# Kernel tuning notes

Measured on AMD Instinct MI355X. Metric: run time of the kernel, lower is better.

## Reference

```python
import jax, jax.numpy as jnp
import numpy as np

N_P, E_P = 50000, 400000
N_L, E_L = 50000, 400000
B = 256  # number of graphs per side
NEG_GAT = 0.2   # GATv2 leaky-relu slope
NEG_FC = 0.01   # nn.LeakyReLU default slope


def _gatv2(x, ei, Wl, Wr, att, b, H, C):
    """GATv2Conv (concat heads, add_self_loops=True). Wl/Wr: [in, H*C], att: [H, C], b: [H*C]."""
    N = x.shape[0]
    sl = jnp.arange(N)
    src = jnp.concatenate([ei[0], sl])
    dst = jnp.concatenate([ei[1], sl])
    xl = (x @ Wl).reshape(N, H, C)   # source transform (messages)
    xr = (x @ Wr).reshape(N, H, C)   # target transform
    e = jax.nn.leaky_relu(xl[src] + xr[dst], NEG_GAT)          # [E+N, H, C]
    logits = jnp.einsum('ehc,hc->eh', e, att)                   # [E+N, H]
    m = jax.ops.segment_max(logits, dst, num_segments=N)        # segment softmax
    a = jnp.exp(logits - m[dst])
    alpha = a / jax.ops.segment_sum(a, dst, num_segments=N)[dst]
    out = jax.ops.segment_sum(xl[src] * alpha[..., None], dst, num_segments=N)
    return out.reshape(N, H * C) + b


def _mean_pool(x, batch, nb):
    s = jax.ops.segment_sum(x, batch, num_segments=nb)
    c = jax.ops.segment_sum(jnp.ones((x.shape[0],), x.dtype), batch, num_segments=nb)
    return s / jnp.maximum(c, 1.0)[:, None]


def setup_inputs() -> dict:
    key = jax.random.key(0)
    ks = jax.random.split(key, 48)
    i = [0]
    def nrm(shape, fan_in):
        k = ks[i[0]]; i[0] += 1
        return jax.random.normal(k, shape, jnp.float32) / np.sqrt(fan_in)
    inp = {}
    inp['protein_x'] = jax.random.normal(ks[40], (N_P, 10), jnp.float32)
    inp['ligand_x'] = jax.random.normal(ks[41], (N_L, 5), jnp.float32)
    inp['protein_edge_index'] = jax.random.randint(ks[42], (2, E_P), 0, N_P)
    inp['ligand_edge_index'] = jax.random.randint(ks[43], (2, E_L), 0, N_L)
    inp['protein_batch'] = (jnp.arange(N_P) * B) // N_P  # sorted graph ids, all segments nonempty
    inp['ligand_batch'] = (jnp.arange(N_L) * B) // N_L
    # GATv2 params: layer1 heads=2 out=128, layer2 heads=1 out=256
    inp['p1_Wl'] = nrm((10, 256), 10); inp['p1_Wr'] = nrm((10, 256), 10)
    inp['p1_att'] = nrm((2, 128), 128); inp['p1_b'] = jnp.zeros((256,), jnp.float32)
    inp['p2_Wl'] = nrm((256, 256), 256); inp['p2_Wr'] = nrm((256, 256), 256)
    inp['p2_att'] = nrm((1, 256), 256); inp['p2_b'] = jnp.zeros((256,), jnp.float32)
    inp['l1_Wl'] = nrm((5, 256), 5); inp['l1_Wr'] = nrm((5, 256), 5)
    inp['l1_att'] = nrm((2, 128), 128); inp['l1_b'] = jnp.zeros((256,), jnp.float32)
    inp['l2_Wl'] = nrm((256, 256), 256); inp['l2_Wr'] = nrm((256, 256), 256)
    inp['l2_att'] = nrm((1, 256), 256); inp['l2_b'] = jnp.zeros((256,), jnp.float32)
    # MultiheadAttention(256, 4) params ([in, out] convention)
    inp['Wq'] = nrm((256, 256), 256); inp['bq'] = jnp.zeros((256,), jnp.float32)
    inp['Wk'] = nrm((256, 256), 256); inp['bk'] = jnp.zeros((256,), jnp.float32)
    inp['Wv'] = nrm((256, 256), 256); inp['bv'] = jnp.zeros((256,), jnp.float32)
    inp['Wo'] = nrm((256, 256), 256); inp['bo'] = jnp.zeros((256,), jnp.float32)
    # fc head
    inp['fc1_w'] = nrm((512, 256), 512); inp['fc1_b'] = jnp.zeros((256,), jnp.float32)
    inp['ln_g'] = jnp.ones((256,), jnp.float32); inp['ln_b'] = jnp.zeros((256,), jnp.float32)
    inp['fc2_w'] = nrm((256, 1), 256); inp['fc2_b'] = jnp.zeros((1,), jnp.float32)
    return inp


def reference(protein_x, protein_edge_index, protein_batch,
              ligand_x, ligand_edge_index, ligand_batch,
              p1_Wl, p1_Wr, p1_att, p1_b, p2_Wl, p2_Wr, p2_att, p2_b,
              l1_Wl, l1_Wr, l1_att, l1_b, l2_Wl, l2_Wr, l2_att, l2_b,
              Wq, bq, Wk, bk, Wv, bv, Wo, bo,
              fc1_w, fc1_b, ln_g, ln_b, fc2_w, fc2_b):
    px = _gatv2(protein_x, protein_edge_index, p1_Wl, p1_Wr, p1_att, p1_b, 2, 128)
    px = _gatv2(px, protein_edge_index, p2_Wl, p2_Wr, p2_att, p2_b, 1, 256)
    px = _mean_pool(px, protein_batch, B)                        # [B, 256]
    lx = _gatv2(ligand_x, ligand_edge_index, l1_Wl, l1_Wr, l1_att, l1_b, 2, 128)
    lx = _gatv2(lx, ligand_edge_index, l2_Wl, l2_Wr, l2_att, l2_b, 1, 256)
    lx = _mean_pool(lx, ligand_batch, B)                         # [B, 256]
    # cross attention with q/k/v seq length 1
    D, H = 256, 4
    d = D // H
    qh = (px @ Wq + bq).reshape(B, H, d)
    kh = (lx @ Wk + bk).reshape(B, H, d)
    vh = (lx @ Wv + bv).reshape(B, H, d)
    scores = (qh * kh).sum(-1) / jnp.sqrt(jnp.float32(d))        # [B, H], 1 key
    w = jax.nn.softmax(scores[..., None], axis=-1)               # all ones (single key)
    attn = (w * vh).reshape(B, D) @ Wo + bo                      # [B, 256]
    comb = jnp.concatenate([px, attn], axis=1)                   # [B, 512]
    h = comb @ fc1_w + fc1_b
    mu = h.mean(-1, keepdims=True)
    var = h.var(-1, keepdims=True)
    h = (h - mu) / jnp.sqrt(var + 1e-5) * ln_g + ln_b
    h = jax.nn.leaky_relu(h, NEG_FC)
    return h @ fc2_w + fc2_b                                     # [B, 1]
```

## Files before the change

kernel.cpp:

```cpp
#include <hip/hip_runtime.h>
#include <math.h>

typedef unsigned short u16;
typedef __attribute__((ext_vector_type(8))) short bf16x8;
typedef __attribute__((ext_vector_type(4))) float f32x4;

__device__ inline u16 f2bf(float x) {
  unsigned int u = __float_as_uint(x);
  u += 0x7fffu + ((u >> 16) & 1u);
  return (u16)(u >> 16);
}
__device__ inline float bf2f(u16 h) {
  return __uint_as_float(((unsigned int)h) << 16);
}
__device__ inline float4 ld_bf4(const u16* p) {
  ushort4 v = *(const ushort4*)p;
  return make_float4(bf2f(v.x), bf2f(v.y), bf2f(v.z), bf2f(v.w));
}

__global__ void k_setup(int* __restrict__ cnt, int nz,
                        const float* __restrict__ Wpl, const float* __restrict__ Wpr,
                        const float* __restrict__ Wll, const float* __restrict__ Wlr,
                        u16* __restrict__ Whp, u16* __restrict__ Wlp,
                        u16* __restrict__ Whl, u16* __restrict__ Wll_o) {
  const int zb = (nz + 255) / 256;
  if ((int)blockIdx.x < zb) {
    int i = blockIdx.x * 256 + threadIdx.x;
    if (i < nz) cnt[i] = 0;
    return;
  }
  int wb = blockIdx.x - zb;
  int n = wb & 511;
  int side = wb >> 9;
  int col = n & 255;
  int k = threadIdx.x;
  const float* W = side == 0 ? (n < 256 ? Wpl : Wpr) : (n < 256 ? Wll : Wlr);
  float w = W[k * 256 + col];
  u16* Wh = side ? Whl : Whp;
  u16* Wlo = side ? Wll_o : Wlp;
  u16 hb = f2bf(w);
  Wh[n * 256 + k] = hb;
  Wlo[n * 256 + k] = f2bf(w - bf2f(hb));
}

__global__ void k_histb(const int* __restrict__ eip, int Ep, const int* __restrict__ eil,
                        int El, int* __restrict__ cntp, int* __restrict__ cntl) {
  int e = blockIdx.x * blockDim.x + threadIdx.x;
  if (e < Ep) atomicAdd(&cntp[eip[Ep + e]], 1);
  else if (e < Ep + El) { int e2 = e - Ep; atomicAdd(&cntl[eil[El + e2]], 1); }
}

__global__ void k_scan1b(const int* __restrict__ cntp, int Np, const int* __restrict__ cntl,
                         int Nl, int nbp, int* __restrict__ offsp, int* __restrict__ offsl,
                         int* __restrict__ curp, int* __restrict__ curl,
                         int* __restrict__ bsum) {
  __shared__ int s[256];
  int tid = threadIdx.x;
  int side = ((int)blockIdx.x >= nbp) ? 1 : 0;
  int blk = side ? (blockIdx.x - nbp) : blockIdx.x;
  const int* cnt = side ? cntl : cntp;
  int* offs = side ? offsl : offsp;
  int* cur = side ? curl : curp;
  int N = side ? Nl : Np;
  int i = blk * 256 + tid;
  int v = (i < N) ? cnt[i] : 0;
  if (i < N) cur[i] = 0;
  s[tid] = v;
  __syncthreads();
  for (int off = 1; off < 256; off <<= 1) {
    int t = 0;
    if (tid >= off) t = s[tid - off];
    __syncthreads();
    if (tid >= off) s[tid] += t;
    __syncthreads();
  }
  if (i < N) offs[i] = s[tid] - v;
  if (tid == 255) bsum[side * 256 + blk] = s[255];
}

__global__ void k_scan2b(int* __restrict__ bsum, int nbp, int nbl) {
  __shared__ int s[256];
  int side = blockIdx.x;
  int nb = side ? nbl : nbp;
  int* bs = bsum + side * 256;
  int tid = threadIdx.x;
  int v = (tid < nb) ? bs[tid] : 0;
  s[tid] = v;
  __syncthreads();
  for (int off = 1; off < 256; off <<= 1) {
    int t = 0;
    if (tid >= off) t = s[tid - off];
    __syncthreads();
    if (tid >= off) s[tid] += t;
    __syncthreads();
  }
  if (tid < nb) bs[tid] = s[tid] - v;
}

__global__ void k_fillb(const int* __restrict__ eip, int Ep, const int* __restrict__ eil,
                        int El, const int* __restrict__ offsp, const int* __restrict__ offsl,
                        const int* __restrict__ bsum,
                        int* __restrict__ curp, int* __restrict__ curl,
                        int* __restrict__ csrp, int* __restrict__ csrl) {
  int e = blockIdx.x * blockDim.x + threadIdx.x;
  if (e < Ep) {
    int d = eip[Ep + e];
    int pos = offsp[d] + bsum[d >> 8] + atomicAdd(&curp[d], 1);
    csrp[pos] = eip[e];
  } else if (e < Ep + El) {
    int e2 = e - Ep;
    int d = eil[El + e2];
    int pos = offsl[d] + bsum[256 + (d >> 8)] + atomicAdd(&curl[d], 1);
    csrl[pos] = eil[e2];
  }
}

__global__ void k_lin_small_b(const float* __restrict__ xp, int Kp, int Np,
                              const float* __restrict__ xl_, int Kl, int Nl,
                              const float* __restrict__ Wpl, const float* __restrict__ Wpr,
                              const float* __restrict__ Wll, const float* __restrict__ Wlr,
                              u16* __restrict__ xlh_p, u16* __restrict__ xrh_p,
                              u16* __restrict__ xlh_l, u16* __restrict__ xrh_l) {
  const int side = blockIdx.y;
  const float* x = side ? xl_ : xp;
  const int K = side ? Kl : Kp;
  const int N = side ? Nl : Np;
  const float* Wl = side ? Wll : Wpl;
  const float* Wr = side ? Wlr : Wpr;
  u16* xlh = side ? xlh_l : xlh_p;
  u16* xrh = side ? xrh_l : xrh_p;
  int base = blockIdx.x * 8;
  if (base >= N) return;
  int j = threadIdx.x;
  __shared__ float xs[8][16];
  int tot = 8 * K;
  for (int i = j; i < tot; i += 256) {
    int r = i / K, k = i - r * K;
    if (base + r < N) xs[r][k] = x[(size_t)(base + r) * K + k];
  }
  __syncthreads();
#pragma unroll
  for (int r = 0; r < 8; ++r) {
    int n = base + r;
    if (n >= N) break;
    float al = 0.f, ar = 0.f;
    for (int k = 0; k < K; ++k) {
      float xv = xs[r][k];
      al = fmaf(xv, Wl[k * 256 + j], al);
      ar = fmaf(xv, Wr[k * 256 + j], ar);
    }
    xlh[(size_t)n * 256 + j] = f2bf(al);
    xrh[(size_t)n * 256 + j] = f2bf(ar);
  }
}

__global__ void __launch_bounds__(256, 2) k_mm_dual_b(
    const u16* __restrict__ A_p, const u16* __restrict__ A_l,
    const u16* __restrict__ Bh_p, const u16* __restrict__ Bl_p,
    const u16* __restrict__ Bh_l, const u16* __restrict__ Bl_l,
    u16* __restrict__ XLh_p, u16* __restrict__ XRh_p,
    u16* __restrict__ XLh_l, u16* __restrict__ XRh_l, int Np, int Nl) {
  __shared__ __align__(16) char smem[32768];
  char* sA = smem;
  char* sBh = smem + 8192;
  char* sBl = smem + 16384;
  const int side = blockIdx.z;
  const u16* A = side ? A_l : A_p;
  const u16* Bhi = side ? Bh_l : Bh_p;
  const u16* Blo = side ? Bl_l : Bl_p;
  u16* XLh = side ? XLh_l : XLh_p;
  u16* XRh = side ? XRh_l : XRh_p;
  const int M = side ? Nl : Np;
  const int t = threadIdx.x;
  const int rowBase = blockIdx.x * 128;
  if (rowBase >= M) return;
  const int j0 = blockIdx.y * 128;
  const int srow = t >> 1;
  const int h = t & 1;
  int gr = rowBase + srow;
  if (gr >= M) gr = M - 1;
  const size_t gaBase = (size_t)gr * 256 + h * 16;
  const size_t gbBase = (size_t)(j0 + srow) * 256 + h * 16;
  const int rb = srow * 64;
  const int sw0 = (((h * 2) + (srow >> 1)) & 3) * 16;
  const int sw1 = (((h * 2 + 1) + (srow >> 1)) & 3) * 16;
  const int lane = t & 63;
  const int wid = t >> 6;
  const int wm = (wid & 1) * 64;
  const int wn = (wid >> 1) * 64;
  const int kq = lane >> 4;
  const int mr = lane & 15;
  int offA[4], offB[4];
#pragma unroll
  for (int i = 0; i < 4; ++i) {
    int m = wm + i * 16 + mr;
    offA[i] = m * 64 + ((kq + (m >> 1)) & 3) * 16;
    int n = wn + i * 16 + mr;
    offB[i] = n * 64 + ((kq + (n >> 1)) & 3) * 16;
  }
  f32x4 acc[4][4] = {};
  for (int kt = 0; kt < 8; ++kt) {
    const int k0 = kt * 32;
    uint4 va0 = *(const uint4*)(A + gaBase + k0);
    uint4 va1 = *(const uint4*)(A + gaBase + k0 + 8);
    uint4 vbh0 = *(const uint4*)(Bhi + gbBase + k0);
    uint4 vbh1 = *(const uint4*)(Bhi + gbBase + k0 + 8);
    uint4 vbl0 = *(const uint4*)(Blo + gbBase + k0);
    uint4 vbl1 = *(const uint4*)(Blo + gbBase + k0 + 8);
    __syncthreads();
    *(uint4*)(sA + rb + sw0) = va0;
    *(uint4*)(sA + rb + sw1) = va1;
    *(uint4*)(sBh + rb + sw0) = vbh0;
    *(uint4*)(sBh + rb + sw1) = vbh1;
    *(uint4*)(sBl + rb + sw0) = vbl0;
    *(uint4*)(sBl + rb + sw1) = vbl1;
    __syncthreads();
    bf16x8 a[4], bh[4], bl[4];
#pragma unroll
    for (int i = 0; i < 4; ++i) {
      a[i] = *(const bf16x8*)(sA + offA[i]);
      bh[i] = *(const bf16x8*)(sBh + offB[i]);
      bl[i] = *(const bf16x8*)(sBl + offB[i]);
    }
#pragma unroll
    for (int i = 0; i < 4; ++i)
#pragma unroll
      for (int j = 0; j < 4; ++j) {
        acc[i][j] = __builtin_amdgcn_mfma_f32_16x16x32_bf16(a[i], bh[j], acc[i][j], 0, 0, 0);
        acc[i][j] = __builtin_amdgcn_mfma_f32_16x16x32_bf16(a[i], bl[j], acc[i][j], 0, 0, 0);
      }
  }
  __syncthreads();
  u16* wtile = (u16*)(smem + wid * 8192);
#pragma unroll
  for (int i = 0; i < 4; ++i)
#pragma unroll
    for (int j = 0; j < 4; ++j)
#pragma unroll
      for (int r = 0; r < 4; ++r)
        wtile[(i * 16 + kq * 4 + r) * 64 + j * 16 + mr] = f2bf(acc[i][j][r]);
  u16* cbase = (blockIdx.y < 2) ? XLh : XRh;
  const int cb = (blockIdx.y < 2) ? j0 : j0 - 256;
  const int r8 = lane >> 3;
  const int c8 = lane & 7;
#pragma unroll
  for (int rr = 0; rr < 8; ++rr) {
    int lr = rr * 8 + r8;
    uint4 v = *(const uint4*)&wtile[lr * 64 + c8 * 8];
    int row = rowBase + wm + lr;
    if (row < M) *(uint4*)&cbase[(size_t)row * 256 + cb + wn + c8 * 8] = v;
  }
}

#define GAT_DOT(a, q)                                                          \
  {                                                                            \
    float t0 = a.x + rd.x, t1 = a.y + rd.y, t2 = a.z + rd.z, t3 = a.w + rd.w;  \
    q = fmaf(t3, wa6.w, fabsf(t3) * wa4.w);                                    \
    q = fmaf(fabsf(t2), wa4.z, fmaf(t2, wa6.z, q));                            \
    q = fmaf(fabsf(t1), wa4.y, fmaf(t1, wa6.y, q));                            \
    q = fmaf(fabsf(t0), wa4.x, fmaf(t0, wa6.x, q));                            \
  }

template <int H>
__global__ void k_gat_gather_b(
    const u16* __restrict__ xlh_p, const u16* __restrict__ xrh_p, u16* __restrict__ out_p,
    const u16* __restrict__ xlh_l, const u16* __restrict__ xrh_l, u16* __restrict__ out_l,
    const int* __restrict__ csr_p, const int* __restrict__ offs_p,
    const int* __restrict__ cnt_p,
    const int* __restrict__ csr_l, const int* __restrict__ offs_l,
    const int* __restrict__ cnt_l, const int* __restrict__ bsum,
    const float* __restrict__ att_p, const float* __restrict__ bias_p,
    const float* __restrict__ att_l, const float* __restrict__ bias_l,
    int Np, int Nl) {
  const int side = blockIdx.y;
  const u16* xlh = side ? xlh_l : xlh_p;
  const u16* xrh = side ? xrh_l : xrh_p;
  u16* out = side ? out_l : out_p;
  const int* csr = side ? csr_l : csr_p;
  const int* offs = side ? offs_l : offs_p;
  const int* cnt = side ? cnt_l : cnt_p;
  const float* att = side ? att_l : att_p;
  const float* bias = side ? bias_l : bias_p;
  const int N = side ? Nl : Np;
  int d = blockIdx.x * 4 + (threadIdx.x >> 6);
  if (d >= N) return;
  const int lo4 = (threadIdx.x & 63) * 4;
  const float4 rd = ld_bf4(&xrh[(size_t)d * 256 + lo4]);
  const float4 wa = *(const float4*)&att[lo4];
  const float4 wa6 = make_float4(0.6f * wa.x, 0.6f * wa.y, 0.6f * wa.z, 0.6f * wa.w);
  const float4 wa4 = make_float4(0.4f * wa.x, 0.4f * wa.y, 0.4f * wa.z, 0.4f * wa.w);
  const float4 xd = ld_bf4(&xlh[(size_t)d * 256 + lo4]);
  float base;
  GAT_DOT(xd, base)
#pragma unroll
  for (int off = 1; off <= (H == 2 ? 16 : 32); off <<= 1) base += __shfl_xor(base, off, 64);
  float l0 = 1.f, l1 = 0.f, l2 = 0.f, l3 = 0.f;
  float4 acc0 = xd;
  float4 acc1 = make_float4(0.f, 0.f, 0.f, 0.f);
  float4 acc2 = make_float4(0.f, 0.f, 0.f, 0.f);
  float4 acc3 = make_float4(0.f, 0.f, 0.f, 0.f);
  const int o0 = offs[d] + bsum[side * 256 + (d >> 8)];
  const int c = cnt[d];
  int j = 0;
  for (; j + 3 < c; j += 4) {
    int s0 = csr[o0 + j], s1 = csr[o0 + j + 1], s2 = csr[o0 + j + 2], s3 = csr[o0 + j + 3];
    float4 a0 = ld_bf4(&xlh[(size_t)s0 * 256 + lo4]);
    float4 a1 = ld_bf4(&xlh[(size_t)s1 * 256 + lo4]);
    float4 a2 = ld_bf4(&xlh[(size_t)s2 * 256 + lo4]);
    float4 a3 = ld_bf4(&xlh[(size_t)s3 * 256 + lo4]);
    float q0, q1, q2, q3;
    GAT_DOT(a0, q0)
    GAT_DOT(a1, q1)
    GAT_DOT(a2, q2)
    GAT_DOT(a3, q3)
#pragma unroll
    for (int off = 1; off <= (H == 2 ? 16 : 32); off <<= 1) {
      q0 += __shfl_xor(q0, off, 64);
      q1 += __shfl_xor(q1, off, 64);
      q2 += __shfl_xor(q2, off, 64);
      q3 += __shfl_xor(q3, off, 64);
    }
    float w0 = __expf(q0 - base), w1 = __expf(q1 - base);
    float w2 = __expf(q2 - base), w3 = __expf(q3 - base);
    l0 += w0; l1 += w1; l2 += w2; l3 += w3;
    acc0.x = fmaf(w0, a0.x, acc0.x); acc0.y = fmaf(w0, a0.y, acc0.y);
    acc0.z = fmaf(w0, a0.z, acc0.z); acc0.w = fmaf(w0, a0.w, acc0.w);
    acc1.x = fmaf(w1, a1.x, acc1.x); acc1.y = fmaf(w1, a1.y, acc1.y);
    acc1.z = fmaf(w1, a1.z, acc1.z); acc1.w = fmaf(w1, a1.w, acc1.w);
    acc2.x = fmaf(w2, a2.x, acc2.x); acc2.y = fmaf(w2, a2.y, acc2.y);
    acc2.z = fmaf(w2, a2.z, acc2.z); acc2.w = fmaf(w2, a2.w, acc2.w);
    acc3.x = fmaf(w3, a3.x, acc3.x); acc3.y = fmaf(w3, a3.y, acc3.y);
    acc3.z = fmaf(w3, a3.z, acc3.z); acc3.w = fmaf(w3, a3.w, acc3.w);
  }
  for (; j < c; ++j) {
    int s0 = csr[o0 + j];
    float4 a0 = ld_bf4(&xlh[(size_t)s0 * 256 + lo4]);
    float q0;
    GAT_DOT(a0, q0)
#pragma unroll
    for (int off = 1; off <= (H == 2 ? 16 : 32); off <<= 1) q0 += __shfl_xor(q0, off, 64);
    float w0 = __expf(q0 - base);
    l0 += w0;
    acc0.x = fmaf(w0, a0.x, acc0.x); acc0.y = fmaf(w0, a0.y, acc0.y);
    acc0.z = fmaf(w0, a0.z, acc0.z); acc0.w = fmaf(w0, a0.w, acc0.w);
  }
  float inv = 1.f / (l0 + l1 + l2 + l3);
  float ax = acc0.x + acc1.x + acc2.x + acc3.x;
  float ay = acc0.y + acc1.y + acc2.y + acc3.y;
  float az = acc0.z + acc1.z + acc2.z + acc3.z;
  float aw = acc0.w + acc1.w + acc2.w + acc3.w;
  const float4 b4 = *(const float4*)&bias[lo4];
  ushort4 hv;
  hv.x = f2bf(ax * inv + b4.x);
  hv.y = f2bf(ay * inv + b4.y);
  hv.z = f2bf(az * inv + b4.z);
  hv.w = f2bf(aw * inv + b4.w);
  *(ushort4*)&out[(size_t)d * 256 + lo4] = hv;
}

#define POOL_C 8
__global__ void k_pool_part(const u16* __restrict__ xp, const int* __restrict__ bp, int Np,
                            const u16* __restrict__ xl_, const int* __restrict__ bl_, int Nl,
                            float* __restrict__ PPpart, float* __restrict__ LPpart) {
  const int b = blockIdx.x;
  const int side = blockIdx.y;
  const int chunk = blockIdx.z;
  const u16* x = side ? xl_ : xp;
  const int* batch = side ? bl_ : bp;
  const int N = side ? Nl : Np;
  float* part = side ? LPpart : PPpart;
  int j = threadIdx.x;
  __shared__ int sss, sse;
  if (j == 0) {
    int lo = 0, hi = N;
    while (lo < hi) { int mid = (lo + hi) >> 1; if (batch[mid] < b) lo = mid + 1; else hi = mid; }
    sss = lo;
    lo = 0; hi = N;
    while (lo < hi) { int mid = (lo + hi) >> 1; if (batch[mid] < b + 1) lo = mid + 1; else hi = mid; }
    sse = lo;
  }
  __syncthreads();
  int len = sse - sss;
  int per = (len + POOL_C - 1) / POOL_C;
  int st = sss + chunk * per;
  int en = st + per;
  if (en > sse) en = sse;
  float acc = 0.f;
  for (int n = st; n < en; ++n) acc += bf2f(x[(size_t)n * 256 + j]);
  part[((size_t)chunk * 256 + b) * 256 + j] = acc;
}

__global__ void k_head(const float* __restrict__ PPpart, const float* __restrict__ LPpart,
                       const int* __restrict__ bp, int Np,
                       const int* __restrict__ bl_, int Nl,
                       const float* __restrict__ Wv, const float* __restrict__ bv,
                       const float* __restrict__ Wo, const float* __restrict__ bo,
                       const float* __restrict__ fc1w, const float* __restrict__ fc1b,
                       const float* __restrict__ lng, const float* __restrict__ lnb,
                       const float* __restrict__ fc2w, const float* __restrict__ fc2b,
                       float* __restrict__ out) {
  int b = blockIdx.x;
  int j = threadIdx.x;
  __shared__ float lxs[256];
  __shared__ float vbuf[256];
  __shared__ float comb[512];
  __shared__ float r1[256], r2[256];
  __shared__ float smu, srs;
  __shared__ int seg[4];
  if (j < 2) {
    const int* batch = j ? bl_ : bp;
    int N = j ? Nl : Np;
    int lo = 0, hi = N;
    while (lo < hi) { int mid = (lo + hi) >> 1; if (batch[mid] < b) lo = mid + 1; else hi = mid; }
    seg[j * 2] = lo;
    lo = 0; hi = N;
    while (lo < hi) { int mid = (lo + hi) >> 1; if (batch[mid] < b + 1) lo = mid + 1; else hi = mid; }
    seg[j * 2 + 1] = lo;
  }
  __syncthreads();
  {
    float accp = 0.f, accl = 0.f;
#pragma unroll
    for (int c = 0; c < POOL_C; ++c) {
      accp += PPpart[((size_t)c * 256 + b) * 256 + j];
      accl += LPpart[((size_t)c * 256 + b) * 256 + j];
    }
    comb[j] = accp / fmaxf((float)(seg[1] - seg[0]), 1.f);
    lxs[j] = accl / fmaxf((float)(seg[3] - seg[2]), 1.f);
  }
  __syncthreads();
  float v = bv[j];
  for (int k = 0; k < 256; ++k) v = fmaf(lxs[k], Wv[k * 256 + j], v);
  vbuf[j] = v;
  __syncthreads();
  float at = bo[j];
  for (int k = 0; k < 256; ++k) at = fmaf(vbuf[k], Wo[k * 256 + j], at);
  comb[256 + j] = at;
  __syncthreads();
  float h = fc1b[j];
  for (int k = 0; k < 512; ++k) h = fmaf(comb[k], fc1w[k * 256 + j], h);
  r1[j] = h;
  r2[j] = h * h;
  __syncthreads();
  for (int off = 128; off > 0; off >>= 1) {
    if (j < off) { r1[j] += r1[j + off]; r2[j] += r2[j + off]; }
    __syncthreads();
  }
  if (j == 0) {
    float mu = r1[0] / 256.f;
    float var = r2[0] / 256.f - mu * mu;
    smu = mu;
    srs = 1.f / sqrtf(var + 1e-5f);
  }
  __syncthreads();
  float hn = (h - smu) * srs * lng[j] + lnb[j];
  hn = hn > 0.f ? hn : 0.01f * hn;
  r1[j] = hn * fc2w[j];
  __syncthreads();
  for (int off = 128; off > 0; off >>= 1) {
    if (j < off) r1[j] += r1[j + off];
    __syncthreads();
  }
  if (j == 0) out[b] = r1[0] + fc2b[0];
}

extern "C" void kernel_launch(void* const* d_in, const int* in_sizes, int n_in,
                              void* d_out, int out_size, void* d_ws, size_t ws_size,
                              hipStream_t stream) {
  const float* px = (const float*)d_in[0];
  const float* lx = (const float*)d_in[1];
  const int* pei = (const int*)d_in[2];
  const int* lei = (const int*)d_in[3];
  const int* pb = (const int*)d_in[4];
  const int* lb = (const int*)d_in[5];
  const float* p1_Wl = (const float*)d_in[6];
  const float* p1_Wr = (const float*)d_in[7];
  const float* p1_att = (const float*)d_in[8];
  const float* p1_b = (const float*)d_in[9];
  const float* p2_Wl = (const float*)d_in[10];
  const float* p2_Wr = (const float*)d_in[11];
  const float* p2_att = (const float*)d_in[12];
  const float* p2_b = (const float*)d_in[13];
  const float* l1_Wl = (const float*)d_in[14];
  const float* l1_Wr = (const float*)d_in[15];
  const float* l1_att = (const float*)d_in[16];
  const float* l1_b = (const float*)d_in[17];
  const float* l2_Wl = (const float*)d_in[18];
  const float* l2_Wr = (const float*)d_in[19];
  const float* l2_att = (const float*)d_in[20];
  const float* l2_b = (const float*)d_in[21];
  const float* Wv = (const float*)d_in[26];
  const float* bv = (const float*)d_in[27];
  const float* Wo = (const float*)d_in[28];
  const float* bo = (const float*)d_in[29];
  const float* fc1w = (const float*)d_in[30];
  const float* fc1b = (const float*)d_in[31];
  const float* lng = (const float*)d_in[32];
  const float* lnb = (const float*)d_in[33];
  const float* fc2w = (const float*)d_in[34];
  const float* fc2b = (const float*)d_in[35];

  const int NPn = in_sizes[4];
  const int NLn = in_sizes[5];
  const int EPe = in_sizes[2] / 2;
  const int ELe = in_sizes[3] / 2;
  const int KP = in_sizes[0] / NPn;
  const int KL = in_sizes[1] / NLn;

  const int Nmax = NPn > NLn ? NPn : NLn;
  const int Emax = EPe > ELe ? EPe : ELe;
  size_t NF = (size_t)Nmax * 256;

  u16* XLh_p = (u16*)d_ws;
  u16* XRh_p = XLh_p + NF;
  u16* Ah_p = XRh_p + NF;
  u16* XLh_l = Ah_p + NF;
  u16* XRh_l = XLh_l + NF;
  u16* Ah_l = XRh_l + NF;
  u16* Wth = Ah_l + NF;
  u16* Wtl = Wth + 2 * 512 * 256;
  float* PPpart = (float*)(Wtl + 2 * 512 * 256);
  float* LPpart = PPpart + (size_t)POOL_C * 256 * 256;
  int* cnt = (int*)(LPpart + (size_t)POOL_C * 256 * 256);
  int* cur = cnt + 2 * (size_t)Nmax;
  int* offs = cur + 2 * (size_t)Nmax;
  int* bsum = offs + 2 * (size_t)Nmax;
  int* csr = bsum + 512;
  int* cnt_l = cnt + Nmax;
  int* cur_l = cur + Nmax;
  int* offs_l = offs + Nmax;
  int* csr_l = csr + Emax;

  const int nbp = (NPn + 255) / 256;
  const int nbl = (NLn + 255) / 256;
  const int nz = 2 * Nmax;
  const int zb = (nz + 255) / 256;

  k_setup<<<zb + 1024, 256, 0, stream>>>(cnt, nz, p2_Wl, p2_Wr, l2_Wl, l2_Wr,
                                         Wth, Wtl, Wth + 512 * 256, Wtl + 512 * 256);
  k_histb<<<(EPe + ELe + 255) / 256, 256, 0, stream>>>(pei, EPe, lei, ELe, cnt, cnt_l);
  k_scan1b<<<nbp + nbl, 256, 0, stream>>>(cnt, NPn, cnt_l, NLn, nbp, offs, offs_l,
                                          cur, cur_l, bsum);
  k_scan2b<<<2, 256, 0, stream>>>(bsum, nbp, nbl);
  k_fillb<<<(EPe + ELe + 255) / 256, 256, 0, stream>>>(pei, EPe, lei, ELe, offs, offs_l,
                                                       bsum, cur, cur_l, csr, csr_l);
  k_lin_small_b<<<dim3((Nmax + 7) / 8, 2), 256, 0, stream>>>(
      px, KP, NPn, lx, KL, NLn, p1_Wl, p1_Wr, l1_Wl, l1_Wr,
      XLh_p, XRh_p, XLh_l, XRh_l);
  k_gat_gather_b<2><<<dim3((Nmax + 3) / 4, 2), 256, 0, stream>>>(
      XLh_p, XRh_p, Ah_p, XLh_l, XRh_l, Ah_l,
      csr, offs, cnt, csr_l, offs_l, cnt_l, bsum,
      p1_att, p1_b, l1_att, l1_b, NPn, NLn);
  k_mm_dual_b<<<dim3((Nmax + 127) / 128, 4, 2), 256, 0, stream>>>(
      Ah_p, Ah_l, Wth, Wtl, Wth + 512 * 256, Wtl + 512 * 256,
      XLh_p, XRh_p, XLh_l, XRh_l, NPn, NLn);
  k_gat_gather_b<1><<<dim3((Nmax + 3) / 4, 2), 256, 0, stream>>>(
      XLh_p, XRh_p, Ah_p, XLh_l, XRh_l, Ah_l,
      csr, offs, cnt, csr_l, offs_l, cnt_l, bsum,
      p2_att, p2_b, l2_att, l2_b, NPn, NLn);
  k_pool_part<<<dim3(256, 2, POOL_C), 256, 0, stream>>>(Ah_p, pb, NPn, Ah_l, lb, NLn,
                                                        PPpart, LPpart);
  k_head<<<256, 256, 0, stream>>>(PPpart, LPpart, pb, NPn, lb, NLn,
                                  Wv, bv, Wo, bo, fc1w, fc1b, lng, lnb, fc2w, fc2b,
                                  (float*)d_out);
  (void)n_in; (void)out_size; (void)ws_size;
}
```

Baseline: 573.8 us.

## Fold layer-1 linear into setup kernel and group GEMM blocks for L2 reuse

Merges the small first-layer linear transform into the setup kernel as extra blocks, which removes one kernel launch. The dual GEMM launch changes from a 3D grid to a flat grid. Groups of 8 row tiles now share their 4 column tiles within 32 consecutive block ids, so A rows and B columns are reused from L2 while hot, and both sides share one padded row range. The trade-off is a larger, more divergent setup kernel and some index arithmetic in the GEMM.

```diff
diff --git a/kernel.cpp b/kernel.cpp
--- a/kernel.cpp
+++ b/kernel.cpp
@@ -19,10 +19,17 @@
 }
 
 __global__ void k_setup(int* __restrict__ cnt, int nz,
-                        const float* __restrict__ Wpl, const float* __restrict__ Wpr,
-                        const float* __restrict__ Wll, const float* __restrict__ Wlr,
+                        const float* __restrict__ W2pl, const float* __restrict__ W2pr,
+                        const float* __restrict__ W2ll, const float* __restrict__ W2lr,
                         u16* __restrict__ Whp, u16* __restrict__ Wlp,
-                        u16* __restrict__ Whl, u16* __restrict__ Wll_o) {
+                        u16* __restrict__ Whl, u16* __restrict__ Wll_o,
+                        const float* __restrict__ xp, int Kp, int Np,
+                        const float* __restrict__ xl_, int Kl, int Nl,
+                        const float* __restrict__ W1pl, const float* __restrict__ W1pr,
+                        const float* __restrict__ W1ll, const float* __restrict__ W1lr,
+                        u16* __restrict__ xlh_p, u16* __restrict__ xrh_p,
+                        u16* __restrict__ xlh_l, u16* __restrict__ xrh_l,
+                        int linPer) {
   const int zb = (nz + 255) / 256;
   if ((int)blockIdx.x < zb) {
     int i = blockIdx.x * 256 + threadIdx.x;
@@ -30,17 +37,52 @@
     return;
   }
   int wb = blockIdx.x - zb;
-  int n = wb & 511;
-  int side = wb >> 9;
-  int col = n & 255;
-  int k = threadIdx.x;
-  const float* W = side == 0 ? (n < 256 ? Wpl : Wpr) : (n < 256 ? Wll : Wlr);
-  float w = W[k * 256 + col];
-  u16* Wh = side ? Whl : Whp;
-  u16* Wlo = side ? Wll_o : Wlp;
-  u16 hb = f2bf(w);
-  Wh[n * 256 + k] = hb;
-  Wlo[n * 256 + k] = f2bf(w - bf2f(hb));
+  if (wb < 1024) {
+    int n = wb & 511;
+    int side = wb >> 9;
+    int col = n & 255;
+    int k = threadIdx.x;
+    const float* W = side == 0 ? (n < 256 ? W2pl : W2pr) : (n < 256 ? W2ll : W2lr);
+    float w = W[k * 256 + col];
+    u16* Wh = side ? Whl : Whp;
+    u16* Wlo = side ? Wll_o : Wlp;
+    u16 hb = f2bf(w);
+    Wh[n * 256 + k] = hb;
+    Wlo[n * 256 + k] = f2bf(w - bf2f(hb));
+    return;
+  }
+  int wb2 = wb - 1024;
+  const int side = wb2 / linPer;
+  const float* x = side ? xl_ : xp;
+  const int K = side ? Kl : Kp;
+  const int N = side ? Nl : Np;
+  const float* Wl = side ? W1ll : W1pl;
+  const float* Wr = side ? W1lr : W1pr;
+  u16* xlh = side ? xlh_l : xlh_p;
+  u16* xrh = side ? xrh_l : xrh_p;
+  int base = (wb2 - side * linPer) * 8;
+  if (base >= N) return;
+  int j = threadIdx.x;
+  __shared__ float xs[8][16];
+  int tot = 8 * K;
+  for (int i = j; i < tot; i += 256) {
+    int r = i / K, k = i - r * K;
+    if (base + r < N) xs[r][k] = x[(size_t)(base + r) * K + k];
+  }
+  __syncthreads();
+#pragma unroll
+  for (int r = 0; r < 8; ++r) {
+    int n = base + r;
+    if (n >= N) break;
+    float al = 0.f, ar = 0.f;
+    for (int k = 0; k < K; ++k) {
+      float xv = xs[r][k];
+      al = fmaf(xv, Wl[k * 256 + j], al);
+      ar = fmaf(xv, Wr[k * 256 + j], ar);
+    }
+    xlh[(size_t)n * 256 + j] = f2bf(al);
+    xrh[(size_t)n * 256 + j] = f2bf(ar);
+  }
 }
 
 __global__ void k_histb(const int* __restrict__ eip, int Ep, const int* __restrict__ eil,
@@ -115,56 +157,22 @@
   }
 }
 
-__global__ void k_lin_small_b(const float* __restrict__ xp, int Kp, int Np,
-                              const float* __restrict__ xl_, int Kl, int Nl,
-                              const float* __restrict__ Wpl, const float* __restrict__ Wpr,
-                              const float* __restrict__ Wll, const float* __restrict__ Wlr,
-                              u16* __restrict__ xlh_p, u16* __restrict__ xrh_p,
-                              u16* __restrict__ xlh_l, u16* __restrict__ xrh_l) {
-  const int side = blockIdx.y;
-  const float* x = side ? xl_ : xp;
-  const int K = side ? Kl : Kp;
-  const int N = side ? Nl : Np;
-  const float* Wl = side ? Wll : Wpl;
-  const float* Wr = side ? Wlr : Wpr;
-  u16* xlh = side ? xlh_l : xlh_p;
-  u16* xrh = side ? xrh_l : xrh_p;
-  int base = blockIdx.x * 8;
-  if (base >= N) return;
-  int j = threadIdx.x;
-  __shared__ float xs[8][16];
-  int tot = 8 * K;
-  for (int i = j; i < tot; i += 256) {
-    int r = i / K, k = i - r * K;
-    if (base + r < N) xs[r][k] = x[(size_t)(base + r) * K + k];
-  }
-  __syncthreads();
-#pragma unroll
-  for (int r = 0; r < 8; ++r) {
-    int n = base + r;
-    if (n >= N) break;
-    float al = 0.f, ar = 0.f;
-    for (int k = 0; k < K; ++k) {
-      float xv = xs[r][k];
-      al = fmaf(xv, Wl[k * 256 + j], al);
-      ar = fmaf(xv, Wr[k * 256 + j], ar);
-    }
-    xlh[(size_t)n * 256 + j] = f2bf(al);
-    xrh[(size_t)n * 256 + j] = f2bf(ar);
-  }
-}
-
 __global__ void __launch_bounds__(256, 2) k_mm_dual_b(
     const u16* __restrict__ A_p, const u16* __restrict__ A_l,
     const u16* __restrict__ Bh_p, const u16* __restrict__ Bl_p,
     const u16* __restrict__ Bh_l, const u16* __restrict__ Bl_l,
     u16* __restrict__ XLh_p, u16* __restrict__ XRh_p,
-    u16* __restrict__ XLh_l, u16* __restrict__ XRh_l, int Np, int Nl) {
+    u16* __restrict__ XLh_l, u16* __restrict__ XRh_l, int Np, int Nl, int Rp, int Rtot) {
   __shared__ __align__(16) char smem[32768];
   char* sA = smem;
   char* sBh = smem + 8192;
   char* sBl = smem + 16384;
-  const int side = blockIdx.z;
+  const int gid = blockIdx.x;
+  const int rblk = (gid >> 5) * 8 + (gid & 7);
+  const int col = (gid >> 3) & 3;
+  if (rblk >= Rtot) return;
+  const int side = (rblk >= Rp) ? 1 : 0;
+  const int rloc = side ? rblk - Rp : rblk;
   const u16* A = side ? A_l : A_p;
   const u16* Bhi = side ? Bh_l : Bh_p;
   const u16* Blo = side ? Bl_l : Bl_p;
@@ -172,9 +180,8 @@
   u16* XRh = side ? XRh_l : XRh_p;
   const int M = side ? Nl : Np;
   const int t = threadIdx.x;
-  const int rowBase = blockIdx.x * 128;
-  if (rowBase >= M) return;
-  const int j0 = blockIdx.y * 128;
+  const int rowBase = rloc * 128;
+  const int j0 = col * 128;
   const int srow = t >> 1;
   const int h = t & 1;
   int gr = rowBase + srow;
@@ -239,8 +246,8 @@
 #pragma unroll
       for (int r = 0; r < 4; ++r)
         wtile[(i * 16 + kq * 4 + r) * 64 + j * 16 + mr] = f2bf(acc[i][j][r]);
-  u16* cbase = (blockIdx.y < 2) ? XLh : XRh;
-  const int cb = (blockIdx.y < 2) ? j0 : j0 - 256;
+  u16* cbase = (col < 2) ? XLh : XRh;
+  const int cb = (col < 2) ? j0 : j0 - 256;
   const int r8 = lane >> 3;
   const int c8 = lane & 7;
 #pragma unroll
@@ -535,25 +542,31 @@
   const int nbl = (NLn + 255) / 256;
   const int nz = 2 * Nmax;
   const int zb = (nz + 255) / 256;
-
-  k_setup<<<zb + 1024, 256, 0, stream>>>(cnt, nz, p2_Wl, p2_Wr, l2_Wl, l2_Wr,
-                                         Wth, Wtl, Wth + 512 * 256, Wtl + 512 * 256);
+  const int linPer = (Nmax + 7) / 8;
+
+  k_setup<<<zb + 1024 + 2 * linPer, 256, 0, stream>>>(
+      cnt, nz, p2_Wl, p2_Wr, l2_Wl, l2_Wr,
+      Wth, Wtl, Wth + 512 * 256, Wtl + 512 * 256,
+      px, KP, NPn, lx, KL, NLn, p1_Wl, p1_Wr, l1_Wl, l1_Wr,
+      XLh_p, XRh_p, XLh_l, XRh_l, linPer);
   k_histb<<<(EPe + ELe + 255) / 256, 256, 0, stream>>>(pei, EPe, lei, ELe, cnt, cnt_l);
   k_scan1b<<<nbp + nbl, 256, 0, stream>>>(cnt, NPn, cnt_l, NLn, nbp, offs, offs_l,
                                           cur, cur_l, bsum);
   k_scan2b<<<2, 256, 0, stream>>>(bsum, nbp, nbl);
   k_fillb<<<(EPe + ELe + 255) / 256, 256, 0, stream>>>(pei, EPe, lei, ELe, offs, offs_l,
                                                        bsum, cur, cur_l, csr, csr_l);
-  k_lin_small_b<<<dim3((Nmax + 7) / 8, 2), 256, 0, stream>>>(
-      px, KP, NPn, lx, KL, NLn, p1_Wl, p1_Wr, l1_Wl, l1_Wr,
-      XLh_p, XRh_p, XLh_l, XRh_l);
   k_gat_gather_b<2><<<dim3((Nmax + 3) / 4, 2), 256, 0, stream>>>(
       XLh_p, XRh_p, Ah_p, XLh_l, XRh_l, Ah_l,
       csr, offs, cnt, csr_l, offs_l, cnt_l, bsum,
       p1_att, p1_b, l1_att, l1_b, NPn, NLn);
-  k_mm_dual_b<<<dim3((Nmax + 127) / 128, 4, 2), 256, 0, stream>>>(
-      Ah_p, Ah_l, Wth, Wtl, Wth + 512 * 256, Wtl + 512 * 256,
-      XLh_p, XRh_p, XLh_l, XRh_l, NPn, NLn);
+  {
+    const int Rp = (NPn + 127) / 128;
+    const int Rl = (NLn + 127) / 128;
+    const int Rtot = Rp + Rl;
+    k_mm_dual_b<<<32 * ((Rtot + 7) / 8), 256, 0, stream>>>(
+        Ah_p, Ah_l, Wth, Wtl, Wth + 512 * 256, Wtl + 512 * 256,
+        XLh_p, XRh_p, XLh_l, XRh_l, NPn, NLn, Rp, Rtot);
+  }
   k_gat_gather_b<1><<<dim3((Nmax + 3) / 4, 2), 256, 0, stream>>>(
       XLh_p, XRh_p, Ah_p, XLh_l, XRh_l, Ah_l,
       csr, offs, cnt, csr_l, offs_l, cnt_l, bsum,
```

Result: no change. 569.3 us (-0.8%).
